# Optimization experiments

Hardware: AMD Instinct MI355X
Metric: run time of the kernel (lower is better)

Reference implementation:

```python
import jax, jax.numpy as jnp
import numpy as np
from jax import lax

MD = 4  # correlation max displacement -> (2*MD+1)**2 = 81 channels
BACKWARP_COEF = 1.25  # level 4 entry in the coefficient table


def leaky(x):
    return jnp.where(x >= 0, x, 0.1 * x)


def conv3x3(x, w, b):
    # x: [B,Cin,H,W], w: [Cout,Cin,3,3]
    y = lax.conv_general_dilated(x, w, (1, 1), [(1, 1), (1, 1)],
                                 dimension_numbers=('NCHW', 'OIHW', 'NCHW'))
    return y + b[None, :, None, None]


def deconv4x4_s2(x, w, b):
    # torch ConvTranspose2d(k=4, s=2, p=1); w: [Cin,Cout,4,4]
    y = lax.conv_general_dilated(x, w[:, :, ::-1, ::-1], (1, 1), [(2, 2), (2, 2)],
                                 lhs_dilation=(2, 2),
                                 dimension_numbers=('NCHW', 'IOHW', 'NCHW'))
    return y + b[None, :, None, None]


def grid_sample_zeros(img, grid):
    # bilinear, padding_mode='zeros', align_corners=False
    B, C, H, W = img.shape
    x = (grid[..., 0] + 1.0) * 0.5 * W - 0.5  # [B,H,W]
    y = (grid[..., 1] + 1.0) * 0.5 * H - 0.5
    x0 = jnp.floor(x); y0 = jnp.floor(y)
    wx1 = x - x0; wx0 = 1.0 - wx1
    wy1 = y - y0; wy0 = 1.0 - wy1

    def gather(ix, iy):
        valid = (ix >= 0) & (ix < W) & (iy >= 0) & (iy < H)
        ixc = jnp.clip(ix, 0, W - 1).astype(jnp.int32)
        iyc = jnp.clip(iy, 0, H - 1).astype(jnp.int32)
        v = jax.vmap(lambda im, yy, xx: im[:, yy, xx])(img, iyc, ixc)  # [B,C,H,W]
        return jnp.where(valid[:, None], v, 0.0)

    out = (gather(x0, y0) * (wx0 * wy0)[:, None]
           + gather(x0 + 1, y0) * (wx1 * wy0)[:, None]
           + gather(x0, y0 + 1) * (wx0 * wy1)[:, None]
           + gather(x0 + 1, y0 + 1) * (wx1 * wy1)[:, None])
    return out


def backwarp(feat, flow):
    B, C, H, W = feat.shape
    gx = jnp.linspace(-1.0 + 1.0 / W, 1.0 - 1.0 / W, W, dtype=feat.dtype)
    gy = jnp.linspace(-1.0 + 1.0 / H, 1.0 - 1.0 / H, H, dtype=feat.dtype)
    fx = flow[:, 0] / ((W - 1.0) / 2.0)
    fy = flow[:, 1] / ((H - 1.0) / 2.0)
    grid = jnp.stack([gx[None, None, :] + fx, gy[None, :, None] + fy], axis=-1)  # [B,H,W,2]
    feat1 = jnp.concatenate([feat, jnp.ones((B, 1, H, W), feat.dtype)], axis=1)
    out = grid_sample_zeros(feat1, grid)
    mask = jnp.where(out[:, -1:] > 0.999, 1.0, 0.0).astype(feat.dtype)
    return out[:, :-1] * mask


def correlation(f1, f2):
    # PWC-Net cost volume: mean over channels of shifted products, 81 shifts
    B, C, H, W = f1.shape
    f2p = jnp.pad(f2, ((0, 0), (0, 0), (MD, MD), (MD, MD)))
    outs = []
    for dy in range(2 * MD + 1):
        for dx in range(2 * MD + 1):
            outs.append(jnp.mean(f1 * f2p[:, :, dy:dy + H, dx:dx + W], axis=1))
    return jnp.stack(outs, axis=1)  # [B,81,H,W]


def setup_inputs() -> dict:
    key = jax.random.key(0)
    ks = jax.random.split(key, 24)
    B, C, H, W = 16, 48, 64, 128
    cc = 81 + 48 + 2 + 2  # 133
    prev_feat_c = 81 + 48 + 48 + 24 + 16  # 217
    p = lambda k, s: jax.random.normal(k, s, dtype=jnp.float32) * 0.05
    return {
        'feat_1': jax.random.normal(ks[0], (B, C, H, W), dtype=jnp.float32),
        'feat_2': jax.random.normal(ks[1], (B, C, H, W), dtype=jnp.float32),
        'prev_flow': jax.random.normal(ks[2], (B, 2, H // 2, W // 2), dtype=jnp.float32),
        'prev_feat': jax.random.normal(ks[3], (B, prev_feat_c, H // 2, W // 2), dtype=jnp.float32),
        'w1': p(ks[4], (48, cc, 3, 3)), 'b1': p(ks[5], (48,)),
        'w2': p(ks[6], (48, cc + 48, 3, 3)), 'b2': p(ks[7], (48,)),
        'w3': p(ks[8], (24, cc + 96, 3, 3)), 'b3': p(ks[9], (24,)),
        'w4': p(ks[10], (16, cc + 120, 3, 3)), 'b4': p(ks[11], (16,)),
        'w5': p(ks[12], (2, cc + 136, 3, 3)), 'b5': p(ks[13], (2,)),
        'w_upflow': p(ks[14], (2, 2, 4, 4)), 'b_upflow': p(ks[15], (2,)),
        'w_upfeat': p(ks[16], (prev_feat_c, 2, 4, 4)), 'b_upfeat': p(ks[17], (2,)),
    }


def reference(feat_1, feat_2, prev_flow, prev_feat,
              w1, b1, w2, b2, w3, b3, w4, b4, w5, b5,
              w_upflow, b_upflow, w_upfeat, b_upfeat):
    upped_flow = deconv4x4_s2(prev_flow, w_upflow, b_upflow)   # [B,2,H,W]
    upped_feat = deconv4x4_s2(prev_feat, w_upfeat, b_upfeat)   # [B,2,H,W]
    warped_feat_2 = backwarp(feat_2, upped_flow * BACKWARP_COEF)
    corr_volume = leaky(correlation(feat_1, warped_feat_2))    # [B,81,H,W]
    feat_out = jnp.concatenate([corr_volume, feat_1, upped_flow, upped_feat], axis=1)
    feat_out = jnp.concatenate([leaky(conv3x3(feat_out, w1, b1)), feat_out], axis=1)
    feat_out = jnp.concatenate([leaky(conv3x3(feat_out, w2, b2)), feat_out], axis=1)
    feat_out = jnp.concatenate([leaky(conv3x3(feat_out, w3, b3)), feat_out], axis=1)
    feat_out = jnp.concatenate([leaky(conv3x3(feat_out, w4, b4)), feat_out], axis=1)
    flow = leaky(conv3x3(feat_out, w5, b5))
    return flow, feat_out
```

## Files before the change

### kernel.cpp

```cpp
#include <hip/hip_runtime.h>


#define DEVFN __device__ __forceinline__

constexpr int B = 16, H = 64, W = 128, HW = H * W;
constexpr int CF = 48;
constexpr int PFC = 217;
constexpr int H2 = 32, W2 = 64, HW2 = H2 * W2;
constexpr int FC = 269;
constexpr int FCP = 272;
constexpr int FLOW_ELEMS = B * 2 * HW;

constexpr int OFF_CORR = 136, OFF_F1 = 217, OFF_UF = 265, OFF_UPFEAT = 267;
constexpr int FB_F1 = 136, FB_CORR = 184;

constexpr size_t WS_ZEROS = 0;
constexpr size_t WS_FEATB = 256;
constexpr size_t FEATB_BYTES = (size_t)B * HW * FCP * 2;
constexpr size_t WS_WARPEDH = WS_FEATB + FEATB_BYTES;
constexpr size_t WARPEDH_BYTES = (size_t)3 * B * HW * 16 * 2;
constexpr size_t WS_PART = WS_WARPEDH + WARPEDH_BYTES;
constexpr size_t PART_BYTES = (size_t)7 * B * 2 * HW * 4;
constexpr size_t WS_WB = WS_PART + PART_BYTES;

typedef short bf16x8 __attribute__((ext_vector_type(8)));
typedef float f32x4 __attribute__((ext_vector_type(4)));
typedef _Float16 h16x2 __attribute__((ext_vector_type(2)));
typedef _Float16 h16x8 __attribute__((ext_vector_type(8)));

DEVFN float leaky(float x) { return x >= 0.f ? x : 0.1f * x; }

DEVFN unsigned short f2b(float f) {
  unsigned int u = __float_as_uint(f);
  u += 0x7FFFu + ((u >> 16) & 1u);
  return (unsigned short)(u >> 16);
}

DEVFN void gload16(const void* g, void* l) {
  __builtin_amdgcn_global_load_lds(
      (const __attribute__((address_space(1))) void*)g,
      (__attribute__((address_space(3))) void*)l, 16, 0, 0);
}

DEVFN int featb2ref(int p) {
  if (p >= FB_F1 && p < FB_CORR) return OFF_F1 + (p - FB_F1);
  if (p >= FB_CORR && p < 265) return OFF_CORR + (p - FB_CORR);
  return p;
}

__global__ __launch_bounds__(256) void k_repack_all(
    const float* __restrict__ w1, const float* __restrict__ w2,
    const float* __restrict__ w3, const float* __restrict__ w4,
    const float* __restrict__ w5,
    unsigned short* __restrict__ wb1, unsigned short* __restrict__ wb2,
    unsigned short* __restrict__ wb3, unsigned short* __restrict__ wb4,
    unsigned short* __restrict__ wb5, unsigned short* __restrict__ zeros) {
  int blk = blockIdx.x;
  if (blk == 0 && threadIdx.x < 32) zeros[threadIdx.x] = 0;
  const float* w;
  unsigned short* wb;
  int CIN, COUT, COUTP, IN_OFF, rbase;
  if (blk < 270)       { w = w1; wb = wb1; CIN = 133; COUT = 48; COUTP = 48; IN_OFF = 136; rbase = 0; }
  else if (blk < 594)  { w = w2; wb = wb2; CIN = 181; COUT = 48; COUTP = 48; IN_OFF = 88;  rbase = 270; }
  else if (blk < 882)  { w = w3; wb = wb3; CIN = 229; COUT = 24; COUTP = 32; IN_OFF = 40;  rbase = 594; }
  else if (blk < 1026) { w = w4; wb = wb4; CIN = 253; COUT = 16; COUTP = 16; IN_OFF = 16;  rbase = 882; }
  else                 { w = w5; wb = wb5; CIN = 269; COUT = 2;  COUTP = 16; IN_OFF = 0;   rbase = 1026; }
  int e = (blk - rbase) * 256 + threadIdx.x;
  int nchunk = (CIN + 31) >> 5;
  int TOT = nchunk * 9 * COUTP * 32;
  if (e >= TOT) return;
  int j = e & 7, qpos = (e >> 3) & 3;
  int row = e >> 5;
  int co = row % COUTP;
  int tapch = row / COUTP;
  int tap = tapch % 9, ch = tapch / 9;
  int k = ch * 32 + ((qpos ^ ((co >> 1) & 3)) << 3) + j;
  float v = 0.f;
  if (co < COUT && k < CIN) {
    int ci = featb2ref(IN_OFF + k) - IN_OFF;
    v = w[(co * CIN + ci) * 9 + tap];
  }
  wb[e] = f2b(v);
}

__global__ __launch_bounds__(256) void k_dcf_dflow(
    const float* __restrict__ pfeat, const float* __restrict__ wup,
    const float* __restrict__ pflow, const float* __restrict__ wuf,
    const float* __restrict__ buf_, float* __restrict__ partial,
    float* __restrict__ feat, unsigned short* __restrict__ featb) {
  __shared__ float wl[1024];
  __shared__ float red[2048];
  int tid = threadIdx.x;
  if (blockIdx.x >= 3584) {
    int t = (blockIdx.x - 3584) * 256 + tid;
    if (t >= B * 2 * HW) return;
    int x = t % W, y = (t / W) % H, co = (t / HW) % 2, b = t / (2 * HW);
    float acc = buf_[co];
    int ky0 = ((y & 1) == 0) ? 1 : 0;
    int kx0 = ((x & 1) == 0) ? 1 : 0;
#pragma unroll
    for (int kyi = 0; kyi < 2; ++kyi) {
      int ky = ky0 + 2 * kyi;
      int iy = (y + 1 - ky) >> 1;
      if (iy < 0 || iy >= H2) continue;
#pragma unroll
      for (int kxi = 0; kxi < 2; ++kxi) {
        int kx = kx0 + 2 * kxi;
        int ix = (x + 1 - kx) >> 1;
        if (ix < 0 || ix >= W2) continue;
#pragma unroll
        for (int ci = 0; ci < 2; ++ci)
          acc += pflow[(b * 2 + ci) * HW2 + iy * W2 + ix] *
                 wuf[((ci * 2 + co) * 4 + ky) * 4 + kx];
      }
    }
    int pix = (b * H + y) * W + x;
    feat[(b * FC + OFF_UF + co) * HW + y * W + x] = acc;
    featb[pix * FCP + OFF_UF + co] = f2b(acc);
    if (co == 0) {
      featb[pix * FCP + 269] = 0;
      featb[pix * FCP + 270] = 0;
      featb[pix * FCP + 271] = 0;
    }
    return;
  }
  int blk = blockIdx.x;
  int chunk = blk % 7, t2 = blk / 7;
  int y2 = t2 % H2, b = t2 / H2;
  int ch0 = chunk * 32;
  for (int i = tid; i < 1024; i += 256) {
    int ci = ch0 + (i >> 5);
    wl[i] = (ci < PFC) ? wup[ci * 32 + (i & 31)] : 0.f;
  }
  __syncthreads();
  int x2 = tid & 63, cg = tid >> 6;
  float acc[8];
#pragma unroll
  for (int v = 0; v < 8; ++v) acc[v] = 0.f;
#pragma unroll 1
  for (int k = 0; k < 8; ++k) {
    int cil = cg * 8 + k;
    int ci = ch0 + cil;
    bool cv = ci < PFC;
    const float* src = pfeat + ((size_t)b * PFC + ci) * HW2;
    float iv[3][3];
#pragma unroll
    for (int dy = -1; dy <= 1; ++dy)
#pragma unroll
      for (int dx = -1; dx <= 1; ++dx) {
        int iy = y2 + dy, ix = x2 + dx;
        float v = 0.f;
        if (cv && iy >= 0 && iy < H2 && ix >= 0 && ix < W2) v = src[iy * W2 + ix];
        iv[dy + 1][dx + 1] = v;
      }
    const float* wc = &wl[cil * 32];
#pragma unroll
    for (int co = 0; co < 2; ++co)
#pragma unroll
      for (int ry = 0; ry < 2; ++ry)
#pragma unroll
        for (int rx = 0; rx < 2; ++rx) {
          float s = acc[co * 4 + ry * 2 + rx];
#pragma unroll
          for (int dy = ry - 1; dy <= ry; ++dy) {
            int ky = 1 + ry - 2 * dy;
#pragma unroll
            for (int dx = rx - 1; dx <= rx; ++dx) {
              int kx = 1 + rx - 2 * dx;
              s += iv[dy + 1][dx + 1] * wc[co * 16 + ky * 4 + kx];
            }
          }
          acc[co * 4 + ry * 2 + rx] = s;
        }
  }
#pragma unroll
  for (int v = 0; v < 8; ++v) red[(cg * 64 + x2) * 8 + v] = acc[v];
  __syncthreads();
  for (int idx = tid; idx < 512; idx += 256) {
    int x2b = idx & 63, vi = idx >> 6;
    float s = red[(0 + x2b) * 8 + vi] + red[(64 + x2b) * 8 + vi] +
              red[(128 + x2b) * 8 + vi] + red[(192 + x2b) * 8 + vi];
    int co = vi >> 2, ry = (vi >> 1) & 1, rx = vi & 1;
    partial[(size_t)chunk * (B * 2 * HW) + (size_t)(b * 2 + co) * HW +
            (2 * y2 + ry) * W + (2 * x2b + rx)] = s;
  }
}

__global__ __launch_bounds__(256) void k_fin_backwarp(
    const float* __restrict__ partial, const float* __restrict__ bup,
    const float* __restrict__ feat2, float* __restrict__ feat,
    unsigned short* __restrict__ featb, unsigned short* __restrict__ warpedh) {
  int tid = threadIdx.x;
  if (blockIdx.x < 1024) {
    int t = blockIdx.x * 256 + tid;
    float s = 0.f;
#pragma unroll
    for (int c = 0; c < 7; ++c) s += partial[(size_t)c * (B * 2 * HW) + t];
    int rem = t % HW;
    int co = (t / HW) & 1;
    int b = t / (2 * HW);
    s += bup[co];
    feat[((size_t)b * FC + OFF_UPFEAT + co) * HW + rem] = s;
    featb[((size_t)(b * H) * W + rem) * FCP + OFF_UPFEAT + co] = f2b(s);
    return;
  }
  int t = (blockIdx.x - 1024) * 256 + tid;
  if (t >= B * HW) return;
  int x = t % W, y = (t / W) % H, b = t / HW;
  const float SX = 1.25f * (float)W / (float)(W - 1);
  const float SY = 1.25f * (float)H / (float)(H - 1);
  float fx = feat[(b * FC + OFF_UF + 0) * HW + y * W + x];
  float fy = feat[(b * FC + OFF_UF + 1) * HW + y * W + x];
  float px = (float)x + fx * SX;
  float py = (float)y + fy * SY;
  float x0f = floorf(px), y0f = floorf(py);
  int ix0 = (int)x0f, iy0 = (int)y0f;
  float wx1 = px - x0f, wx0 = 1.f - wx1;
  float wy1 = py - y0f, wy0 = 1.f - wy1;
  bool vx0 = (ix0 >= 0) & (ix0 < W), vx1 = (ix0 + 1 >= 0) & (ix0 + 1 < W);
  bool vy0 = (iy0 >= 0) & (iy0 < H), vy1 = (iy0 + 1 >= 0) & (iy0 + 1 < H);
  float w00 = (vx0 && vy0) ? wx0 * wy0 : 0.f;
  float w01 = (vx1 && vy0) ? wx1 * wy0 : 0.f;
  float w10 = (vx0 && vy1) ? wx0 * wy1 : 0.f;
  float w11 = (vx1 && vy1) ? wx1 * wy1 : 0.f;
  float wsum = w00 + w01 + w10 + w11;
  float m = wsum > 0.999f ? 1.f : 0.f;
  w00 *= m; w01 *= m; w10 *= m; w11 *= m;
  int cx0 = min(max(ix0, 0), W - 1), cx1 = min(max(ix0 + 1, 0), W - 1);
  int cy0 = min(max(iy0, 0), H - 1), cy1 = min(max(iy0 + 1, 0), H - 1);
  const float* s = feat2 + b * CF * HW;
  int o00 = cy0 * W + cx0, o01 = cy0 * W + cx1, o10 = cy1 * W + cx0, o11 = cy1 * W + cx1;
#pragma unroll 1
  for (int chunk = 0; chunk < 3; ++chunk) {
    h16x8 out0, out1;
#pragma unroll
    for (int k = 0; k < 16; ++k) {
      const float* sc = s + (chunk * 16 + k) * HW;
      float v = w00 * sc[o00] + w01 * sc[o01] + w10 * sc[o10] + w11 * sc[o11];
      if (k < 8) out0[k & 7] = (_Float16)v;
      else       out1[k & 7] = (_Float16)v;
    }
    h16x8* dst = (h16x8*)(warpedh + ((size_t)chunk * B * HW + t) * 16);
    dst[0] = out0;
    dst[1] = out1;
  }
}

__global__ __launch_bounds__(256) void k_corr(const float* __restrict__ f1,
                                              const unsigned short* __restrict__ warpedh,
                                              const unsigned short* __restrict__ zeros,
                                              float* __restrict__ feat,
                                              unsigned short* __restrict__ featb) {
  __shared__ __align__(16) unsigned short lds[5 * 136 * 16];
  const int swz = ((blockIdx.x & 7) << 7) | (blockIdx.x >> 3);
  const int y = swz & 63, b = swz >> 6;
  const int tid = threadIdx.x;
  const int px = tid >> 1, h = tid & 1;
  const int lane = tid & 63, wv = tid >> 6;
  const int pix = (b * H + y) * W + px;
  const h16x8* hp = (const h16x8*)lds;
  char* ldsc = (char*)lds;
  const float inv = 1.f / 48.f;

#pragma unroll 1
  for (int half = 0; half < 2; ++half) {
    const int R = half ? 4 : 5;
    const int dybase = half ? 5 : 0;
    const int ND = R * 9;
    float acc[45];
#pragma unroll
    for (int d = 0; d < 45; ++d) acc[d] = 0.f;
#pragma unroll 1
    for (int chunk = 0; chunk < 3; ++chunk) {
      __syncthreads();
      const int NQ = R * 136 * 2;
      for (int q0 = 0; q0 < NQ; q0 += 256) {
        int q = q0 + tid;
        if (q < NQ) {
          int pr = q >> 1, u = q & 1;
          int r = pr / 136, p = pr - r * 136;
          int sw = (p >> 2) & 1;
          int yy = y + dybase + r - 4, xx = p - 4;
          const unsigned short* src = zeros;
          if (yy >= 0 && yy < H && xx >= 0 && xx < W)
            src = warpedh + (((size_t)chunk * B * H + b * H + yy) * W + xx) * 16 +
                  (u ^ sw) * 8;
          gload16(src, ldsc + (size_t)q0 * 16 + wv * 1024 + lane * 16);
        }
      }
      float av[8];
      const int c0 = chunk * 16 + h * 8;
#pragma unroll
      for (int j = 0; j < 8; ++j)
        av[j] = f1[((size_t)b * CF + c0 + j) * HW + y * W + px];
      h16x2 fh[4];
#pragma unroll
      for (int j = 0; j < 4; ++j) {
        fh[j][0] = (_Float16)av[2 * j];
        fh[j][1] = (_Float16)av[2 * j + 1];
      }
      asm volatile("s_waitcnt vmcnt(0)" ::: "memory");
      __syncthreads();
      if (half == 0) {
#pragma unroll
        for (int j = 0; j < 8; ++j)
          feat[((size_t)b * FC + OFF_F1 + c0 + j) * HW + y * W + px] = av[j];
        uint4 qv;
        qv.x = (unsigned)f2b(av[0]) | ((unsigned)f2b(av[1]) << 16);
        qv.y = (unsigned)f2b(av[2]) | ((unsigned)f2b(av[3]) << 16);
        qv.z = (unsigned)f2b(av[4]) | ((unsigned)f2b(av[5]) << 16);
        qv.w = (unsigned)f2b(av[6]) | ((unsigned)f2b(av[7]) << 16);
        *(uint4*)(featb + (size_t)pix * FCP + FB_F1 + c0) = qv;
      }
#pragma unroll
      for (int dy = 0; dy < 5; ++dy) {
        if (dy < R) {
#pragma unroll
          for (int dx = 0; dx < 9; ++dx) {
            int p = px + dx;
            int sw = (p >> 2) & 1;
            h16x8 v = hp[((dy * 136 + p) << 1) | (h ^ sw)];
            float a = acc[dy * 9 + dx];
            a = __builtin_amdgcn_fdot2((h16x2){v[0], v[1]}, fh[0], a, false);
            a = __builtin_amdgcn_fdot2((h16x2){v[2], v[3]}, fh[1], a, false);
            a = __builtin_amdgcn_fdot2((h16x2){v[4], v[5]}, fh[2], a, false);
            a = __builtin_amdgcn_fdot2((h16x2){v[6], v[7]}, fh[3], a, false);
            acc[dy * 9 + dx] = a;
          }
        }
      }
    }
#pragma unroll
    for (int d = 0; d < 45; ++d) {
      if (d < ND) {
        float s = acc[d] + __shfl_xor(acc[d], 1);
        acc[d] = leaky(s * inv);
      }
    }
    if (h == 0) {
#pragma unroll
      for (int d = 0; d < 45; ++d)
        if (d < ND)
          feat[((size_t)b * FC + OFF_CORR + dybase * 9 + d) * HW + y * W + px] = acc[d];
    } else {
      unsigned short* fb = featb + (size_t)pix * FCP + FB_CORR + dybase * 9;
      if (half == 0) {
#pragma unroll
        for (int g = 0; g < 5; ++g) {
          uint4 qv;
          qv.x = (unsigned)f2b(acc[8 * g + 0]) | ((unsigned)f2b(acc[8 * g + 1]) << 16);
          qv.y = (unsigned)f2b(acc[8 * g + 2]) | ((unsigned)f2b(acc[8 * g + 3]) << 16);
          qv.z = (unsigned)f2b(acc[8 * g + 4]) | ((unsigned)f2b(acc[8 * g + 5]) << 16);
          qv.w = (unsigned)f2b(acc[8 * g + 6]) | ((unsigned)f2b(acc[8 * g + 7]) << 16);
          *(uint4*)(fb + 8 * g) = qv;
        }
#pragma unroll
        for (int d = 40; d < 45; ++d) fb[d] = f2b(acc[d]);
      } else {
        fb[0] = f2b(acc[0]);
        fb[1] = f2b(acc[1]);
        fb[2] = f2b(acc[2]);
#pragma unroll
        for (int g = 0; g < 4; ++g) {
          uint4 qv;
          qv.x = (unsigned)f2b(acc[3 + 8 * g + 0]) | ((unsigned)f2b(acc[3 + 8 * g + 1]) << 16);
          qv.y = (unsigned)f2b(acc[3 + 8 * g + 2]) | ((unsigned)f2b(acc[3 + 8 * g + 3]) << 16);
          qv.z = (unsigned)f2b(acc[3 + 8 * g + 4]) | ((unsigned)f2b(acc[3 + 8 * g + 5]) << 16);
          qv.w = (unsigned)f2b(acc[3 + 8 * g + 6]) | ((unsigned)f2b(acc[3 + 8 * g + 7]) << 16);
          *(uint4*)(fb + 3 + 8 * g) = qv;
        }
        fb[35] = f2b(acc[35]);
      }
    }
  }
}

template <int CIN, int NCHUNK, int COUT, int COUTP, int IN_OFF, int OUT_OFF, bool TO_FLOW>
__global__ __launch_bounds__(256) void k_conv_mfma(
    const unsigned short* __restrict__ featb, const unsigned short* __restrict__ wb,
    const float* __restrict__ bias, const unsigned short* __restrict__ zeros,
    float* __restrict__ fout, unsigned short* __restrict__ bout) {
  constexpr int NF = COUTP / 16;
  constexpr int ROWPX = 144;
  constexpr int IN_ELE = 4 * ROWPX * 32;
  constexpr int W_SLAB = 9 * COUTP * 32;
  constexpr int NWI = (W_SLAB * 2) / 1024;
  constexpr int CLIM = 264 - IN_OFF;

  __shared__ unsigned short lds[IN_ELE + W_SLAB];

  const int swz = ((blockIdx.x & 7) << 6) | (blockIdx.x >> 3);
  const int y0 = (swz & 31) * 2, b = swz >> 5;
  const int lane = threadIdx.x & 63, wv = threadIdx.x >> 6;
  const int wr = wv >> 1, wc = wv & 1;
  const int arow = lane & 15, aslc = lane >> 4;

  const unsigned short* gp[9];
  int c8a[9];
  int lofs[9];
#pragma unroll
  for (int t = 0; t < 9; ++t) {
    int i = wv + t * 4;
    int r = i / 9, seg = i - r * 9;
    int slot = seg * 16 + (lane >> 2);
    int sub8 = ((lane & 3) ^ ((slot >> 1) & 3)) << 3;
    int yy = y0 + r - 1, xx = slot - 1;
    lofs[t] = (r * ROWPX + seg * 16) * 64;
    gp[t] = zeros; c8a[t] = 1 << 20;
    if (yy >= 0 && yy < H && xx >= 0 && xx < W) {
      gp[t] = featb + ((b * H + yy) * W + xx) * FCP + IN_OFF + sub8;
      c8a[t] = sub8;
    }
  }

  int a_off[4][3];
#pragma unroll
  for (int mi = 0; mi < 4; ++mi)
#pragma unroll
    for (int kx = 0; kx < 3; ++kx) {
      int slot = (wc * 4 + mi) * 16 + arow + kx;
      a_off[mi][kx] = slot * 32 + ((aslc ^ ((slot >> 1) & 3)) << 3);
    }
  int b_off[NF];
#pragma unroll
  for (int nf = 0; nf < NF; ++nf) {
    int co = nf * 16 + arow;
    b_off[nf] = IN_ELE + co * 32 + ((aslc ^ ((co >> 1) & 3)) << 3);
  }

  f32x4 acc[4][NF];
#pragma unroll
  for (int mi = 0; mi < 4; ++mi)
#pragma unroll
    for (int nf = 0; nf < NF; ++nf) acc[mi][nf] = (f32x4){0.f, 0.f, 0.f, 0.f};

  char* ldsc = (char*)lds;

  for (int ch = 0; ch < NCHUNK; ++ch) {
    const int ci0 = ch * 32;
    __syncthreads();
#pragma unroll
    for (int t = 0; t < 9; ++t) {
      const unsigned short* g = (c8a[t] + ci0 <= CLIM) ? gp[t] + ci0 : zeros;
      gload16(g, ldsc + lofs[t]);
    }
    for (int wi = wv; wi < NWI; wi += 4)
      gload16(wb + (size_t)ch * W_SLAB + wi * 512 + lane * 8,
              ldsc + IN_ELE * 2 + wi * 1024);
    asm volatile("s_waitcnt vmcnt(0)" ::: "memory");
    __syncthreads();
#pragma unroll
    for (int ky = 0; ky < 3; ++ky) {
#pragma unroll
      for (int kx = 0; kx < 3; ++kx) {
        bf16x8 afr[4];
#pragma unroll
        for (int mi = 0; mi < 4; ++mi)
          afr[mi] = *(const bf16x8*)(lds + a_off[mi][kx] + (wr + ky) * (ROWPX * 32));
#pragma unroll
        for (int nf = 0; nf < NF; ++nf) {
          bf16x8 bfr = *(const bf16x8*)(lds + b_off[nf] + (ky * 3 + kx) * (COUTP * 32));
#pragma unroll
          for (int mi = 0; mi < 4; ++mi)
            acc[mi][nf] = __builtin_amdgcn_mfma_f32_16x16x32_bf16(
                afr[mi], bfr, acc[mi][nf], 0, 0, 0);
        }
      }
    }
  }

  const int dcol = lane & 15;
  const int yout = y0 + wr;
#pragma unroll
  for (int nf = 0; nf < NF; ++nf) {
    int co = nf * 16 + dcol;
    if (co < COUT) {
      float bv = bias[co];
#pragma unroll
      for (int mi = 0; mi < 4; ++mi) {
#pragma unroll
        for (int r = 0; r < 4; ++r) {
          int pixel = (wc * 4 + mi) * 16 + (lane >> 4) * 4 + r;
          float v = leaky(acc[mi][nf][r] + bv);
          if constexpr (TO_FLOW) {
            fout[(b * 2 + co) * HW + yout * W + pixel] = v;
          } else {
            fout[(b * FC + OUT_OFF + co) * HW + yout * W + pixel] = v;
            bout[((b * H + yout) * W + pixel) * FCP + OUT_OFF + co] = f2b(v);
          }
        }
      }
    }
  }
}

extern "C" void kernel_launch(void* const* d_in, const int* in_sizes, int n_in,
                              void* d_out, int out_size, void* d_ws, size_t ws_size,
                              hipStream_t stream) {
  (void)in_sizes; (void)n_in; (void)out_size; (void)ws_size;
  const float* feat_1 = (const float*)d_in[0];
  const float* feat_2 = (const float*)d_in[1];
  const float* prev_flow = (const float*)d_in[2];
  const float* prev_feat = (const float*)d_in[3];
  const float* w1 = (const float*)d_in[4];
  const float* b1 = (const float*)d_in[5];
  const float* w2 = (const float*)d_in[6];
  const float* b2 = (const float*)d_in[7];
  const float* w3 = (const float*)d_in[8];
  const float* b3 = (const float*)d_in[9];
  const float* w4 = (const float*)d_in[10];
  const float* b4 = (const float*)d_in[11];
  const float* w5 = (const float*)d_in[12];
  const float* b5 = (const float*)d_in[13];
  const float* w_upflow = (const float*)d_in[14];
  const float* b_upflow = (const float*)d_in[15];
  const float* w_upfeat = (const float*)d_in[16];
  const float* b_upfeat = (const float*)d_in[17];

  float* out = (float*)d_out;
  float* feat = out + FLOW_ELEMS;

  char* ws = (char*)d_ws;
  unsigned short* zeros = (unsigned short*)(ws + WS_ZEROS);
  unsigned short* featb = (unsigned short*)(ws + WS_FEATB);
  unsigned short* warpedh = (unsigned short*)(ws + WS_WARPEDH);
  float* partial = (float*)(ws + WS_PART);
  unsigned short* wb1 = (unsigned short*)(ws + WS_WB);
  unsigned short* wb2 = wb1 + 5 * 9 * 48 * 32;
  unsigned short* wb3 = wb2 + 6 * 9 * 48 * 32;
  unsigned short* wb4 = wb3 + 8 * 9 * 32 * 32;
  unsigned short* wb5 = wb4 + 8 * 9 * 16 * 32;

  k_repack_all<<<1188, 256, 0, stream>>>(w1, w2, w3, w4, w5,
                                         wb1, wb2, wb3, wb4, wb5, zeros);
  k_dcf_dflow<<<3584 + 1024, 256, 0, stream>>>(prev_feat, w_upfeat, prev_flow,
                                               w_upflow, b_upflow, partial, feat, featb);
  k_fin_backwarp<<<1024 + 512, 256, 0, stream>>>(partial, b_upfeat, feat_2,
                                                 feat, featb, warpedh);
  k_corr<<<B * H, 256, 0, stream>>>(feat_1, warpedh, zeros, feat, featb);

  k_conv_mfma<133, 5, 48, 48, 136, 88, false><<<B * H / 2, 256, 0, stream>>>(featb, wb1, b1, zeros, feat, featb);
  k_conv_mfma<181, 6, 48, 48, 88, 40, false><<<B * H / 2, 256, 0, stream>>>(featb, wb2, b2, zeros, feat, featb);
  k_conv_mfma<229, 8, 24, 32, 40, 16, false><<<B * H / 2, 256, 0, stream>>>(featb, wb3, b3, zeros, feat, featb);
  k_conv_mfma<253, 8, 16, 16, 16, 0, false><<<B * H / 2, 256, 0, stream>>>(featb, wb4, b4, zeros, feat, featb);
  k_conv_mfma<269, 9, 2, 16, 0, 0, true><<<B * H / 2, 256, 0, stream>>>(featb, wb5, b5, zeros, out, nullptr);
}
```

Measured before the change: 247.7 us.

## Merge weight repack into deconv kernel and split correlation halves across blocks

Folds the weight-repack kernel into the deconvolution kernel as extra leading blocks, which removes one launch and lets the two independent jobs run together. The correlation kernel now launches twice as many blocks, each handling one of the two displacement-row halves instead of looping over both. This raises parallelism and occupancy for the correlation step, at the cost of reloading f1 and re-staging the warped tiles per half. The conv launches are unchanged (B*H/2 = 512).

```diff
diff --git a/kernel.cpp b/kernel.cpp
--- a/kernel.cpp
+++ b/kernel.cpp
@@ -48,51 +48,51 @@
   return p;
 }
 
-__global__ __launch_bounds__(256) void k_repack_all(
+__global__ __launch_bounds__(256) void k_prep(
     const float* __restrict__ w1, const float* __restrict__ w2,
     const float* __restrict__ w3, const float* __restrict__ w4,
     const float* __restrict__ w5,
     unsigned short* __restrict__ wb1, unsigned short* __restrict__ wb2,
     unsigned short* __restrict__ wb3, unsigned short* __restrict__ wb4,
-    unsigned short* __restrict__ wb5, unsigned short* __restrict__ zeros) {
-  int blk = blockIdx.x;
-  if (blk == 0 && threadIdx.x < 32) zeros[threadIdx.x] = 0;
-  const float* w;
-  unsigned short* wb;
-  int CIN, COUT, COUTP, IN_OFF, rbase;
-  if (blk < 270)       { w = w1; wb = wb1; CIN = 133; COUT = 48; COUTP = 48; IN_OFF = 136; rbase = 0; }
-  else if (blk < 594)  { w = w2; wb = wb2; CIN = 181; COUT = 48; COUTP = 48; IN_OFF = 88;  rbase = 270; }
-  else if (blk < 882)  { w = w3; wb = wb3; CIN = 229; COUT = 24; COUTP = 32; IN_OFF = 40;  rbase = 594; }
-  else if (blk < 1026) { w = w4; wb = wb4; CIN = 253; COUT = 16; COUTP = 16; IN_OFF = 16;  rbase = 882; }
-  else                 { w = w5; wb = wb5; CIN = 269; COUT = 2;  COUTP = 16; IN_OFF = 0;   rbase = 1026; }
-  int e = (blk - rbase) * 256 + threadIdx.x;
-  int nchunk = (CIN + 31) >> 5;
-  int TOT = nchunk * 9 * COUTP * 32;
-  if (e >= TOT) return;
-  int j = e & 7, qpos = (e >> 3) & 3;
-  int row = e >> 5;
-  int co = row % COUTP;
-  int tapch = row / COUTP;
-  int tap = tapch % 9, ch = tapch / 9;
-  int k = ch * 32 + ((qpos ^ ((co >> 1) & 3)) << 3) + j;
-  float v = 0.f;
-  if (co < COUT && k < CIN) {
-    int ci = featb2ref(IN_OFF + k) - IN_OFF;
-    v = w[(co * CIN + ci) * 9 + tap];
-  }
-  wb[e] = f2b(v);
-}
-
-__global__ __launch_bounds__(256) void k_dcf_dflow(
+    unsigned short* __restrict__ wb5, unsigned short* __restrict__ zeros,
     const float* __restrict__ pfeat, const float* __restrict__ wup,
     const float* __restrict__ pflow, const float* __restrict__ wuf,
     const float* __restrict__ buf_, float* __restrict__ partial,
     float* __restrict__ feat, unsigned short* __restrict__ featb) {
   __shared__ float wl[1024];
   __shared__ float red[2048];
-  int tid = threadIdx.x;
-  if (blockIdx.x >= 3584) {
-    int t = (blockIdx.x - 3584) * 256 + tid;
+  const int tid = threadIdx.x;
+  const int gblk = blockIdx.x;
+  if (gblk < 1188) {
+    if (gblk == 0 && tid < 32) zeros[tid] = 0;
+    const float* w;
+    unsigned short* wb;
+    int CIN, COUT, COUTP, IN_OFF, rbase;
+    if (gblk < 270)       { w = w1; wb = wb1; CIN = 133; COUT = 48; COUTP = 48; IN_OFF = 136; rbase = 0; }
+    else if (gblk < 594)  { w = w2; wb = wb2; CIN = 181; COUT = 48; COUTP = 48; IN_OFF = 88;  rbase = 270; }
+    else if (gblk < 882)  { w = w3; wb = wb3; CIN = 229; COUT = 24; COUTP = 32; IN_OFF = 40;  rbase = 594; }
+    else if (gblk < 1026) { w = w4; wb = wb4; CIN = 253; COUT = 16; COUTP = 16; IN_OFF = 16;  rbase = 882; }
+    else                  { w = w5; wb = wb5; CIN = 269; COUT = 2;  COUTP = 16; IN_OFF = 0;   rbase = 1026; }
+    int e = (gblk - rbase) * 256 + tid;
+    int nchunk = (CIN + 31) >> 5;
+    int TOT = nchunk * 9 * COUTP * 32;
+    if (e >= TOT) return;
+    int j = e & 7, qpos = (e >> 3) & 3;
+    int row = e >> 5;
+    int co = row % COUTP;
+    int tapch = row / COUTP;
+    int tap = tapch % 9, ch = tapch / 9;
+    int k = ch * 32 + ((qpos ^ ((co >> 1) & 3)) << 3) + j;
+    float v = 0.f;
+    if (co < COUT && k < CIN) {
+      int ci = featb2ref(IN_OFF + k) - IN_OFF;
+      v = w[(co * CIN + ci) * 9 + tap];
+    }
+    wb[e] = f2b(v);
+    return;
+  }
+  if (gblk >= 4772) {
+    int t = (gblk - 4772) * 256 + tid;
     if (t >= B * 2 * HW) return;
     int x = t % W, y = (t / W) % H, co = (t / HW) % 2, b = t / (2 * HW);
     float acc = buf_[co];
@@ -124,7 +124,7 @@
     }
     return;
   }
-  int blk = blockIdx.x;
+  int blk = gblk - 1188;
   int chunk = blk % 7, t2 = blk / 7;
   int y2 = t2 % H2, b = t2 / H2;
   int ch0 = chunk * 32;
@@ -252,8 +252,9 @@
                                               float* __restrict__ feat,
                                               unsigned short* __restrict__ featb) {
   __shared__ __align__(16) unsigned short lds[5 * 136 * 16];
-  const int swz = ((blockIdx.x & 7) << 7) | (blockIdx.x >> 3);
-  const int y = swz & 63, b = swz >> 6;
+  const int swz = ((blockIdx.x & 7) << 8) | (blockIdx.x >> 3);
+  const int half = swz & 1;
+  const int y = (swz >> 1) & 63, b = swz >> 7;
   const int tid = threadIdx.x;
   const int px = tid >> 1, h = tid & 1;
   const int lane = tid & 63, wv = tid >> 6;
@@ -262,115 +263,112 @@
   char* ldsc = (char*)lds;
   const float inv = 1.f / 48.f;
 
+  const int R = half ? 4 : 5;
+  const int dybase = half ? 5 : 0;
+  const int ND = R * 9;
+  float acc[45];
+#pragma unroll
+  for (int d = 0; d < 45; ++d) acc[d] = 0.f;
 #pragma unroll 1
-  for (int half = 0; half < 2; ++half) {
-    const int R = half ? 4 : 5;
-    const int dybase = half ? 5 : 0;
-    const int ND = R * 9;
-    float acc[45];
-#pragma unroll
-    for (int d = 0; d < 45; ++d) acc[d] = 0.f;
-#pragma unroll 1
-    for (int chunk = 0; chunk < 3; ++chunk) {
-      __syncthreads();
-      const int NQ = R * 136 * 2;
-      for (int q0 = 0; q0 < NQ; q0 += 256) {
-        int q = q0 + tid;
-        if (q < NQ) {
-          int pr = q >> 1, u = q & 1;
-          int r = pr / 136, p = pr - r * 136;
+  for (int chunk = 0; chunk < 3; ++chunk) {
+    __syncthreads();
+    const int NQ = R * 136 * 2;
+    for (int q0 = 0; q0 < NQ; q0 += 256) {
+      int q = q0 + tid;
+      if (q < NQ) {
+        int pr = q >> 1, u = q & 1;
+        int r = pr / 136, p = pr - r * 136;
+        int sw = (p >> 2) & 1;
+        int yy = y + dybase + r - 4, xx = p - 4;
+        const unsigned short* src = zeros;
+        if (yy >= 0 && yy < H && xx >= 0 && xx < W)
+          src = warpedh + (((size_t)chunk * B * H + b * H + yy) * W + xx) * 16 +
+                (u ^ sw) * 8;
+        gload16(src, ldsc + (size_t)q0 * 16 + wv * 1024 + lane * 16);
+      }
+    }
+    float av[8];
+    const int c0 = chunk * 16 + h * 8;
+#pragma unroll
+    for (int j = 0; j < 8; ++j)
+      av[j] = f1[((size_t)b * CF + c0 + j) * HW + y * W + px];
+    h16x2 fh[4];
+#pragma unroll
+    for (int j = 0; j < 4; ++j) {
+      fh[j][0] = (_Float16)av[2 * j];
+      fh[j][1] = (_Float16)av[2 * j + 1];
+    }
+    asm volatile("s_waitcnt vmcnt(0)" ::: "memory");
+    __syncthreads();
+    if (half == 0) {
+#pragma unroll
+      for (int j = 0; j < 8; ++j)
+        feat[((size_t)b * FC + OFF_F1 + c0 + j) * HW + y * W + px] = av[j];
+      uint4 qv;
+      qv.x = (unsigned)f2b(av[0]) | ((unsigned)f2b(av[1]) << 16);
+      qv.y = (unsigned)f2b(av[2]) | ((unsigned)f2b(av[3]) << 16);
+      qv.z = (unsigned)f2b(av[4]) | ((unsigned)f2b(av[5]) << 16);
+      qv.w = (unsigned)f2b(av[6]) | ((unsigned)f2b(av[7]) << 16);
+      *(uint4*)(featb + (size_t)pix * FCP + FB_F1 + c0) = qv;
+    }
+#pragma unroll
+    for (int dy = 0; dy < 5; ++dy) {
+      if (dy < R) {
+#pragma unroll
+        for (int dx = 0; dx < 9; ++dx) {
+          int p = px + dx;
           int sw = (p >> 2) & 1;
-          int yy = y + dybase + r - 4, xx = p - 4;
-          const unsigned short* src = zeros;
-          if (yy >= 0 && yy < H && xx >= 0 && xx < W)
-            src = warpedh + (((size_t)chunk * B * H + b * H + yy) * W + xx) * 16 +
-                  (u ^ sw) * 8;
-          gload16(src, ldsc + (size_t)q0 * 16 + wv * 1024 + lane * 16);
+          h16x8 v = hp[((dy * 136 + p) << 1) | (h ^ sw)];
+          float a = acc[dy * 9 + dx];
+          a = __builtin_amdgcn_fdot2((h16x2){v[0], v[1]}, fh[0], a, false);
+          a = __builtin_amdgcn_fdot2((h16x2){v[2], v[3]}, fh[1], a, false);
+          a = __builtin_amdgcn_fdot2((h16x2){v[4], v[5]}, fh[2], a, false);
+          a = __builtin_amdgcn_fdot2((h16x2){v[6], v[7]}, fh[3], a, false);
+          acc[dy * 9 + dx] = a;
         }
       }
-      float av[8];
-      const int c0 = chunk * 16 + h * 8;
-#pragma unroll
-      for (int j = 0; j < 8; ++j)
-        av[j] = f1[((size_t)b * CF + c0 + j) * HW + y * W + px];
-      h16x2 fh[4];
-#pragma unroll
-      for (int j = 0; j < 4; ++j) {
-        fh[j][0] = (_Float16)av[2 * j];
-        fh[j][1] = (_Float16)av[2 * j + 1];
-      }
-      asm volatile("s_waitcnt vmcnt(0)" ::: "memory");
-      __syncthreads();
-      if (half == 0) {
-#pragma unroll
-        for (int j = 0; j < 8; ++j)
-          feat[((size_t)b * FC + OFF_F1 + c0 + j) * HW + y * W + px] = av[j];
+    }
+  }
+#pragma unroll
+  for (int d = 0; d < 45; ++d) {
+    if (d < ND) {
+      float s = acc[d] + __shfl_xor(acc[d], 1);
+      acc[d] = leaky(s * inv);
+    }
+  }
+  if (h == 0) {
+#pragma unroll
+    for (int d = 0; d < 45; ++d)
+      if (d < ND)
+        feat[((size_t)b * FC + OFF_CORR + dybase * 9 + d) * HW + y * W + px] = acc[d];
+  } else {
+    unsigned short* fb = featb + (size_t)pix * FCP + FB_CORR + dybase * 9;
+    if (half == 0) {
+#pragma unroll
+      for (int g = 0; g < 5; ++g) {
         uint4 qv;
-        qv.x = (unsigned)f2b(av[0]) | ((unsigned)f2b(av[1]) << 16);
-        qv.y = (unsigned)f2b(av[2]) | ((unsigned)f2b(av[3]) << 16);
-        qv.z = (unsigned)f2b(av[4]) | ((unsigned)f2b(av[5]) << 16);
-        qv.w = (unsigned)f2b(av[6]) | ((unsigned)f2b(av[7]) << 16);
-        *(uint4*)(featb + (size_t)pix * FCP + FB_F1 + c0) = qv;
-      }
-#pragma unroll
-      for (int dy = 0; dy < 5; ++dy) {
-        if (dy < R) {
-#pragma unroll
-          for (int dx = 0; dx < 9; ++dx) {
-            int p = px + dx;
-            int sw = (p >> 2) & 1;
-            h16x8 v = hp[((dy * 136 + p) << 1) | (h ^ sw)];
-            float a = acc[dy * 9 + dx];
-            a = __builtin_amdgcn_fdot2((h16x2){v[0], v[1]}, fh[0], a, false);
-            a = __builtin_amdgcn_fdot2((h16x2){v[2], v[3]}, fh[1], a, false);
-            a = __builtin_amdgcn_fdot2((h16x2){v[4], v[5]}, fh[2], a, false);
-            a = __builtin_amdgcn_fdot2((h16x2){v[6], v[7]}, fh[3], a, false);
-            acc[dy * 9 + dx] = a;
-          }
-        }
-      }
-    }
-#pragma unroll
-    for (int d = 0; d < 45; ++d) {
-      if (d < ND) {
-        float s = acc[d] + __shfl_xor(acc[d], 1);
-        acc[d] = leaky(s * inv);
-      }
-    }
-    if (h == 0) {
-#pragma unroll
-      for (int d = 0; d < 45; ++d)
-        if (d < ND)
-          feat[((size_t)b * FC + OFF_CORR + dybase * 9 + d) * HW + y * W + px] = acc[d];
+        qv.x = (unsigned)f2b(acc[8 * g + 0]) | ((unsigned)f2b(acc[8 * g + 1]) << 16);
+        qv.y = (unsigned)f2b(acc[8 * g + 2]) | ((unsigned)f2b(acc[8 * g + 3]) << 16);
+        qv.z = (unsigned)f2b(acc[8 * g + 4]) | ((unsigned)f2b(acc[8 * g + 5]) << 16);
+        qv.w = (unsigned)f2b(acc[8 * g + 6]) | ((unsigned)f2b(acc[8 * g + 7]) << 16);
+        *(uint4*)(fb + 8 * g) = qv;
+      }
+#pragma unroll
+      for (int d = 40; d < 45; ++d) fb[d] = f2b(acc[d]);
     } else {
-      unsigned short* fb = featb + (size_t)pix * FCP + FB_CORR + dybase * 9;
-      if (half == 0) {
-#pragma unroll
-        for (int g = 0; g < 5; ++g) {
-          uint4 qv;
-          qv.x = (unsigned)f2b(acc[8 * g + 0]) | ((unsigned)f2b(acc[8 * g + 1]) << 16);
-          qv.y = (unsigned)f2b(acc[8 * g + 2]) | ((unsigned)f2b(acc[8 * g + 3]) << 16);
-          qv.z = (unsigned)f2b(acc[8 * g + 4]) | ((unsigned)f2b(acc[8 * g + 5]) << 16);
-          qv.w = (unsigned)f2b(acc[8 * g + 6]) | ((unsigned)f2b(acc[8 * g + 7]) << 16);
-          *(uint4*)(fb + 8 * g) = qv;
-        }
-#pragma unroll
-        for (int d = 40; d < 45; ++d) fb[d] = f2b(acc[d]);
-      } else {
-        fb[0] = f2b(acc[0]);
-        fb[1] = f2b(acc[1]);
-        fb[2] = f2b(acc[2]);
-#pragma unroll
-        for (int g = 0; g < 4; ++g) {
-          uint4 qv;
-          qv.x = (unsigned)f2b(acc[3 + 8 * g + 0]) | ((unsigned)f2b(acc[3 + 8 * g + 1]) << 16);
-          qv.y = (unsigned)f2b(acc[3 + 8 * g + 2]) | ((unsigned)f2b(acc[3 + 8 * g + 3]) << 16);
-          qv.z = (unsigned)f2b(acc[3 + 8 * g + 4]) | ((unsigned)f2b(acc[3 + 8 * g + 5]) << 16);
-          qv.w = (unsigned)f2b(acc[3 + 8 * g + 6]) | ((unsigned)f2b(acc[3 + 8 * g + 7]) << 16);
-          *(uint4*)(fb + 3 + 8 * g) = qv;
-        }
-        fb[35] = f2b(acc[35]);
-      }
+      fb[0] = f2b(acc[0]);
+      fb[1] = f2b(acc[1]);
+      fb[2] = f2b(acc[2]);
+#pragma unroll
+      for (int g = 0; g < 4; ++g) {
+        uint4 qv;
+        qv.x = (unsigned)f2b(acc[3 + 8 * g + 0]) | ((unsigned)f2b(acc[3 + 8 * g + 1]) << 16);
+        qv.y = (unsigned)f2b(acc[3 + 8 * g + 2]) | ((unsigned)f2b(acc[3 + 8 * g + 3]) << 16);
+        qv.z = (unsigned)f2b(acc[3 + 8 * g + 4]) | ((unsigned)f2b(acc[3 + 8 * g + 5]) << 16);
+        qv.w = (unsigned)f2b(acc[3 + 8 * g + 6]) | ((unsigned)f2b(acc[3 + 8 * g + 7]) << 16);
+        *(uint4*)(fb + 3 + 8 * g) = qv;
+      }
+      fb[35] = f2b(acc[35]);
     }
   }
 }
@@ -531,17 +529,16 @@
   unsigned short* wb4 = wb3 + 8 * 9 * 32 * 32;
   unsigned short* wb5 = wb4 + 8 * 9 * 16 * 32;
 
-  k_repack_all<<<1188, 256, 0, stream>>>(w1, w2, w3, w4, w5,
-                                         wb1, wb2, wb3, wb4, wb5, zeros);
-  k_dcf_dflow<<<3584 + 1024, 256, 0, stream>>>(prev_feat, w_upfeat, prev_flow,
-                                               w_upflow, b_upflow, partial, feat, featb);
+  k_prep<<<1188 + 3584 + 1024, 256, 0, stream>>>(
+      w1, w2, w3, w4, w5, wb1, wb2, wb3, wb4, wb5, zeros,
+      prev_feat, w_upfeat, prev_flow, w_upflow, b_upflow, partial, feat, featb);
   k_fin_backwarp<<<1024 + 512, 256, 0, stream>>>(partial, b_upfeat, feat_2,
                                                  feat, featb, warpedh);
-  k_corr<<<B * H, 256, 0, stream>>>(feat_1, warpedh, zeros, feat, featb);
-
-  k_conv_mfma<133, 5, 48, 48, 136, 88, false><<<B * H / 2, 256, 0, stream>>>(featb, wb1, b1, zeros, feat, featb);
-  k_conv_mfma<181, 6, 48, 48, 88, 40, false><<<B * H / 2, 256, 0, stream>>>(featb, wb2, b2, zeros, feat, featb);
-  k_conv_mfma<229, 8, 24, 32, 40, 16, false><<<B * H / 2, 256, 0, stream>>>(featb, wb3, b3, zeros, feat, featb);
-  k_conv_mfma<253, 8, 16, 16, 16, 0, false><<<B * H / 2, 256, 0, stream>>>(featb, wb4, b4, zeros, feat, featb);
-  k_conv_mfma<269, 9, 2, 16, 0, 0, true><<<B * H / 2, 256, 0, stream>>>(featb, wb5, b5, zeros, out, nullptr);
-}
+  k_corr<<<B * H * 2, 256, 0, stream>>>(feat_1, warpedh, zeros, feat, featb);
+
+  k_conv_mfma<133, 5, 48, 48, 136, 88, false><<<512, 256, 0, stream>>>(featb, wb1, b1, zeros, feat, featb);
+  k_conv_mfma<181, 6, 48, 48, 88, 40, false><<<512, 256, 0, stream>>>(featb, wb2, b2, zeros, feat, featb);
+  k_conv_mfma<229, 8, 24, 32, 40, 16, false><<<512, 256, 0, stream>>>(featb, wb3, b3, zeros, feat, featb);
+  k_conv_mfma<253, 8, 16, 16, 16, 0, false><<<512, 256, 0, stream>>>(featb, wb4, b4, zeros, feat, featb);
+  k_conv_mfma<269, 9, 2, 16, 0, 0, true><<<512, 256, 0, stream>>>(featb, wb5, b5, zeros, out, nullptr);
+}
```

New measurement: 241.7 us (median of 2 runs). 2.4% less time.
